# Performance work log

Hardware: AMD Instinct MI355X
Metric: run time of the kernel (lower is better)

Reference implementation:

```python
import jax, jax.numpy as jnp
import numpy as np
import math

HIDDEN = 2048
N_HEADS = 16
HEAD_DIM = HIDDEN // N_HEADS
BASE = 10000.0


def setup_inputs() -> dict:
    key = jax.random.key(0)
    ks = jax.random.split(key, 8)
    s = 1.0 / math.sqrt(HIDDEN)
    inp = {
        "hidden_states": jax.random.normal(ks[0], (2, 2048, HIDDEN), dtype=jnp.float32),
        "Wq": jax.random.normal(ks[1], (HIDDEN, HIDDEN), dtype=jnp.float32) * s,
        "bq": jax.random.normal(ks[2], (HIDDEN,), dtype=jnp.float32) * s,
        "Wk": jax.random.normal(ks[3], (HIDDEN, HIDDEN), dtype=jnp.float32) * s,
        "bk": jax.random.normal(ks[4], (HIDDEN,), dtype=jnp.float32) * s,
        "Wv": jax.random.normal(ks[5], (HIDDEN, HIDDEN), dtype=jnp.float32) * s,
        "bv": jax.random.normal(ks[6], (HIDDEN,), dtype=jnp.float32) * s,
        "Wo": jax.random.normal(ks[7], (HIDDEN, HIDDEN), dtype=jnp.float32) * s,
    }
    return inp


def _rotate_half(x):
    x1, x2 = x[..., : x.shape[-1] // 2], x[..., x.shape[-1] // 2 :]
    return jnp.concatenate((-x2, x1), axis=-1)


def _rope_cos_sin(seq_len, dtype):
    inv_freq = 1.0 / (BASE ** (jnp.arange(0, HEAD_DIM, 2, dtype=jnp.float32) / HEAD_DIM))
    t = jnp.arange(seq_len, dtype=jnp.float32)
    freqs = jnp.einsum("i,j->ij", t, inv_freq)  # [S, head_dim/2]
    emb = jnp.concatenate((freqs, freqs), axis=-1)  # [S, head_dim]
    return jnp.cos(emb).astype(dtype), jnp.sin(emb).astype(dtype)


def reference(hidden_states, Wq, bq, Wk, bk, Wv, bv, Wo):
    B, S, _ = hidden_states.shape
    q = hidden_states @ Wq + bq
    k = hidden_states @ Wk + bk
    v = hidden_states @ Wv + bv
    # [B, H, S, D]
    q = q.reshape(B, S, N_HEADS, HEAD_DIM).transpose(0, 2, 1, 3)
    k = k.reshape(B, S, N_HEADS, HEAD_DIM).transpose(0, 2, 1, 3)
    v = v.reshape(B, S, N_HEADS, HEAD_DIM).transpose(0, 2, 1, 3)
    cos, sin = _rope_cos_sin(S, q.dtype)  # [S, D]
    cos = cos[None, None]
    sin = sin[None, None]
    q = q * cos + _rotate_half(q) * sin
    k = k * cos + _rotate_half(k) * sin
    scale = 1.0 / math.sqrt(HEAD_DIM)
    scores = jnp.einsum("bhqd,bhkd->bhqk", q, k) * scale
    attn = jax.nn.softmax(scores, axis=-1)
    out = jnp.einsum("bhqk,bhkd->bhqd", attn, v)
    out = out.transpose(0, 2, 1, 3).reshape(B, S, HIDDEN)
    return out @ Wo
```

## Files before the change

kernel.cpp:

```cpp
#include <hip/hip_runtime.h>

#define HID 2048
#define SEQ 2048
#define HD 128
#define QKN 6144

typedef float f32x4 __attribute__((ext_vector_type(4)));
typedef short s16x8 __attribute__((ext_vector_type(8)));
typedef __bf16 bf16x8 __attribute__((ext_vector_type(8)));

static __device__ __forceinline__ unsigned short f2bf(float x) {
    unsigned u = __float_as_uint(x);
    u = u + 0x7FFFu + ((u >> 16) & 1u);
    return (unsigned short)(u >> 16);
}
static __device__ __forceinline__ float bf2f(unsigned short h) {
    return __uint_as_float(((unsigned)h) << 16);
}
static __device__ __forceinline__ bf16x8 as_bf(s16x8 v) {
    union { s16x8 s; bf16x8 b; } u; u.s = v; return u.b;
}
static __device__ __forceinline__ bf16x8 ld_bf8(const unsigned short* p) {
    return as_bf(*(const s16x8*)p);
}
static __device__ __forceinline__ void gload_lds16(const void* g, void* l) {
    __builtin_amdgcn_global_load_lds(
        (const __attribute__((address_space(1))) void*)g,
        (__attribute__((address_space(3))) void*)l,
        16, 0, 0);
}

__global__ __launch_bounds__(256) void fill_f32(
    float* __restrict__ out, float v, int n)
{
    int i = blockIdx.x * 256 + threadIdx.x;
    if (i < n) out[i] = v;
}

__global__ __launch_bounds__(256) void convert_f32_bf16(
    const float* __restrict__ in, unsigned short* __restrict__ out)
{
    long i = ((long)blockIdx.x * 256 + threadIdx.x) * 8;
    f32x4 a = *(const f32x4*)&in[i];
    f32x4 b = *(const f32x4*)&in[i + 4];
    s16x8 o;
#pragma unroll
    for (int e = 0; e < 4; ++e) {
        o[e]     = (short)f2bf(a[e]);
        o[e + 4] = (short)f2bf(b[e]);
    }
    *(s16x8*)&out[i] = o;
}

__global__ __launch_bounds__(256) void transpose_w(
    const float* __restrict__ W, unsigned short* __restrict__ Wt)
{
    __shared__ float t[32][33];
    int k0 = blockIdx.x * 32, n0 = blockIdx.y * 32;
    int tx = threadIdx.x & 31, ty = threadIdx.x >> 5;
#pragma unroll
    for (int r = ty; r < 32; r += 8)
        t[r][tx] = W[(long)(k0 + r) * HID + n0 + tx];
    __syncthreads();
#pragma unroll
    for (int r = ty; r < 32; r += 8)
        Wt[(long)(n0 + r) * HID + k0 + tx] = f2bf(t[tx][r]);
}

template<int NF, bool F32OUT>
__global__ __launch_bounds__(512, 2) void gemm_8phase(
    const unsigned short* __restrict__ A,
    const unsigned short* __restrict__ Bt,
    const float* __restrict__ bq, const float* __restrict__ bk,
    const float* __restrict__ bv,
    unsigned short* __restrict__ Cb, float* __restrict__ Cf,
    int K, int ldc, int nbn, int sm, int sn, int hasBias)
{
    constexpr int BUFE = 16384 + NF * 4096;
    constexpr int SP = (NF + 1) / 2;
    __shared__ unsigned short lds[2 * BUFE];
    const int tid = threadIdx.x;
    const int wid = tid >> 6, lane = tid & 63;
    const int l16 = lane & 15, l4 = lane >> 4;
    const int wm = wid >> 2, wn = wid & 3;

    const int bid = blockIdx.x;
    const int xcd = bid & 7, idx = bid >> 3;
    const int ncn = nbn / sn;
    const int cm = xcd / ncn, cn = xcd % ncn;
    const int lm = idx / sn,  ln = idx % sn;
    const long bm = (long)(cm * sm + lm) * 256;
    const long bn = (long)(cn * sn + ln) * (NF * 64);

    const int NT = K >> 6;
    const long strideB = (long)K * 2;
    const int srow = tid >> 3;
    const int scb  = ((tid & 7) * 16) ^ ((srow & 7) << 4);

    auto stageA = [&](int t, int c) {
        unsigned short* base = &lds[(t & 1) * BUFE];
        const int row = c * 64 + srow;
        const char* src = (const char*)A + (bm + row) * strideB + (long)t * 128 + scb;
        gload_lds16(src, base + (c * 64 + wid * 8) * 64);
    };
    auto stageB = [&](int t, int c) {
        unsigned short* base = &lds[(t & 1) * BUFE + 16384];
        const int row = c * 64 + srow;
        const char* src = (const char*)Bt + (bn + row) * strideB + (long)t * 128 + scb;
        gload_lds16(src, base + (c * 64 + wid * 8) * 64);
    };

    f32x4 acc[8][NF];
#pragma unroll
    for (int i = 0; i < 8; ++i)
#pragma unroll
        for (int j = 0; j < NF; ++j) acc[i][j] = f32x4{0.f, 0.f, 0.f, 0.f};

    auto phase = [&](const unsigned short* Ab, const unsigned short* Bb, int qm, int part) {
        bf16x8 af[4][2];
#pragma unroll
        for (int i = 0; i < 4; ++i) {
            const int row = wm * 128 + (qm * 4 + i) * 16 + l16;
            const char* rb = (const char*)Ab + row * 128;
#pragma unroll
            for (int kk = 0; kk < 2; ++kk)
                af[i][kk] = as_bf(*(const s16x8*)(rb + ((kk * 64 + l4 * 16) ^ ((l16 & 7) << 4))));
        }
        if (part == 0) {
            bf16x8 bfr[SP][2];
#pragma unroll
            for (int j = 0; j < SP; ++j) {
                const int row = wn * (NF * 16) + j * 16 + l16;
                const char* rb = (const char*)Bb + row * 128;
#pragma unroll
                for (int kk = 0; kk < 2; ++kk)
                    bfr[j][kk] = as_bf(*(const s16x8*)(rb + ((kk * 64 + l4 * 16) ^ ((l16 & 7) << 4))));
            }
            __builtin_amdgcn_s_setprio(1);
#pragma unroll
            for (int kk = 0; kk < 2; ++kk)
#pragma unroll
                for (int i = 0; i < 4; ++i)
#pragma unroll
                    for (int j = 0; j < SP; ++j)
                        acc[qm * 4 + i][j] = __builtin_amdgcn_mfma_f32_16x16x32_bf16(
                            af[i][kk], bfr[j][kk], acc[qm * 4 + i][j], 0, 0, 0);
            __builtin_amdgcn_s_setprio(0);
        } else {
            bf16x8 bfr[NF - SP][2];
#pragma unroll
            for (int j = 0; j < NF - SP; ++j) {
                const int row = wn * (NF * 16) + (SP + j) * 16 + l16;
                const char* rb = (const char*)Bb + row * 128;
#pragma unroll
                for (int kk = 0; kk < 2; ++kk)
                    bfr[j][kk] = as_bf(*(const s16x8*)(rb + ((kk * 64 + l4 * 16) ^ ((l16 & 7) << 4))));
            }
            __builtin_amdgcn_s_setprio(1);
#pragma unroll
            for (int kk = 0; kk < 2; ++kk)
#pragma unroll
                for (int i = 0; i < 4; ++i)
#pragma unroll
                    for (int j = 0; j < NF - SP; ++j)
                        acc[qm * 4 + i][SP + j] = __builtin_amdgcn_mfma_f32_16x16x32_bf16(
                            af[i][kk], bfr[j][kk], acc[qm * 4 + i][SP + j], 0, 0, 0);
            __builtin_amdgcn_s_setprio(0);
        }
    };

#pragma unroll
    for (int c = 0; c < 4; ++c) stageA(0, c);
#pragma unroll
    for (int c = 0; c < NF; ++c) stageB(0, c);

    for (int t = 0; t < NT - 1; ++t) {
        const unsigned short* Ab = &lds[(t & 1) * BUFE];
        const unsigned short* Bb = Ab + 16384;
#pragma unroll
        for (int c = 0; c < 4; ++c) stageA(t + 1, c);
        __builtin_amdgcn_sched_barrier(0);
        asm volatile("s_waitcnt vmcnt(4)" ::: "memory");
        __builtin_amdgcn_s_barrier();
        __builtin_amdgcn_sched_barrier(0);
        phase(Ab, Bb, 0, 0);
        __builtin_amdgcn_s_barrier();
#pragma unroll
        for (int c = 0; c < NF; ++c) stageB(t + 1, c);
        phase(Ab, Bb, 0, 1);
        __builtin_amdgcn_s_barrier();
        phase(Ab, Bb, 1, 0);
        __builtin_amdgcn_s_barrier();
        phase(Ab, Bb, 1, 1);
        __builtin_amdgcn_s_barrier();
    }
    {
        const unsigned short* Ab = &lds[((NT - 1) & 1) * BUFE];
        const unsigned short* Bb = Ab + 16384;
        asm volatile("s_waitcnt vmcnt(0)" ::: "memory");
        __builtin_amdgcn_s_barrier();
        __builtin_amdgcn_sched_barrier(0);
        phase(Ab, Bb, 0, 0); __builtin_amdgcn_s_barrier();
        phase(Ab, Bb, 0, 1); __builtin_amdgcn_s_barrier();
        phase(Ab, Bb, 1, 0); __builtin_amdgcn_s_barrier();
        phase(Ab, Bb, 1, 1);
    }

#pragma unroll
    for (int nf = 0; nf < NF; ++nf) {
        const long n = bn + wn * (NF * 16) + nf * 16 + l16;
        float bvv = 0.f;
        if (hasBias)
            bvv = (n < HID) ? bq[n] : ((n < 2 * HID) ? bk[n - HID] : bv[n - 2 * HID]);
#pragma unroll
        for (int mf = 0; mf < 8; ++mf) {
#pragma unroll
            for (int r = 0; r < 4; ++r) {
                const long m = bm + wm * 128 + mf * 16 + l4 * 4 + r;
                float v = acc[mf][nf][r] + bvv;
                if (F32OUT) Cf[m * (long)ldc + n] = v;
                else        Cb[m * (long)ldc + n] = f2bf(v);
            }
        }
    }
}

__global__ __launch_bounds__(256) void rope_kernel(unsigned short* __restrict__ qkv)
{
    int t = blockIdx.x * 256 + threadIdx.x;
    int j8 = t & 7;
    int h  = (t >> 3) & 15;
    int qk = (t >> 7) & 1;
    int row = t >> 8;
    int s = row & (SEQ - 1);
    unsigned short* p = &qkv[(long)row * QKN + qk * HID + h * HD + j8 * 8];
    s16x8 lo = *(const s16x8*)p;
    s16x8 hi = *(const s16x8*)(p + 64);
    float qscale = qk ? 1.0f : 0.08838834764831845f;
    s16x8 olo, ohi;
#pragma unroll
    for (int e = 0; e < 8; ++e) {
        int j = j8 * 8 + e;
        float inv = exp2f(-(float)j * 0.20762050593046f);
        float sn, cs;
        sincosf((float)s * inv, &sn, &cs);
        float x1 = bf2f((unsigned short)lo[e]);
        float x2 = bf2f((unsigned short)hi[e]);
        olo[e] = (short)f2bf((x1 * cs - x2 * sn) * qscale);
        ohi[e] = (short)f2bf((x2 * cs + x1 * sn) * qscale);
    }
    *(s16x8*)p = olo;
    *(s16x8*)(p + 64) = ohi;
}

__global__ __launch_bounds__(256) void v_transpose(
    const unsigned short* __restrict__ qkv, unsigned short* __restrict__ vt)
{
    __shared__ unsigned short t[32][33];
    int bh = blockIdx.z;
    int b = bh >> 4, h = bh & 15;
    int s0 = blockIdx.x * 32, d0 = blockIdx.y * 32;
    int tx = threadIdx.x & 31, ty = threadIdx.x >> 5;
#pragma unroll
    for (int r = ty; r < 32; r += 8)
        t[r][tx] = qkv[(long)(b * SEQ + s0 + r) * QKN + 2 * HID + h * HD + d0 + tx];
    __syncthreads();
#pragma unroll
    for (int r = ty; r < 32; r += 8)
        vt[((long)bh * HD + d0 + r) * SEQ + s0 + tx] = t[tx][r];
}

__global__ __launch_bounds__(512) void attn_kernel(
    const unsigned short* __restrict__ qkv,
    const unsigned short* __restrict__ vt,
    unsigned short* __restrict__ attnout)
{
    __shared__ unsigned short Ks[2][64 * 128];
    __shared__ unsigned short Vs[2][128 * 64];

    const int tid = threadIdx.x, wid = tid >> 6, lane = tid & 63;
    const int l16 = lane & 15, l4 = lane >> 4;
    const int bid = blockIdx.x;
    const int xcd = bid & 7, idx = bid >> 3;
    const int bh = xcd * 4 + (idx >> 4);
    const int qt = idx & 15;
    const int b = bh >> 4, h = bh & 15;
    const long rowbase = (long)b * SEQ;

    const unsigned short* Kg = &qkv[rowbase * QKN + HID + h * HD];
    const unsigned short* Vg = &vt[(long)bh * HD * SEQ];

    auto stage = [&](int buf, int kv0) {
#pragma unroll
        for (int i = 0; i < 2; ++i) {
            int c = wid * 2 + i;
            int kr = c * 4 + l4;
            int kcb = (l16 * 16) ^ ((kr & 7) << 4);
            gload_lds16((const char*)(Kg + (long)(kv0 + kr) * QKN) + kcb, &Ks[buf][c * 512]);
            int vr = c * 8 + (lane >> 3);
            int vcb = ((lane & 7) * 16) ^ ((vr & 7) << 4);
            gload_lds16((const char*)(Vg + (long)vr * SEQ + kv0) + vcb, &Vs[buf][c * 512]);
        }
    };

    bf16x8 qf[4];
    {
        const long qrow = rowbase + qt * 128 + wid * 16 + l16;
        const unsigned short* qp = &qkv[qrow * QKN + h * HD];
#pragma unroll
        for (int kc = 0; kc < 4; ++kc) qf[kc] = ld_bf8(qp + kc * 32 + l4 * 8);
    }

    f32x4 o[8];
#pragma unroll
    for (int nb = 0; nb < 8; ++nb) o[nb] = f32x4{0.f, 0.f, 0.f, 0.f};
    float mrun = -3.0e38f, lrun = 0.f;

    const int srcA = ((l4 & 1) * 2) * 16 + l16;
    const int srcB = srcA + 16;
    const bool sel = (l4 >> 1) != 0;

    stage(0, 0);
    __syncthreads();

    for (int t = 0; t < SEQ / 64; ++t) {
        const int cur = t & 1;
        if (t < SEQ / 64 - 1) stage(cur ^ 1, (t + 1) * 64);
        __builtin_amdgcn_sched_barrier(0);

        const unsigned short* Kc = &Ks[cur][0];
        const unsigned short* Vc = &Vs[cur][0];

        f32x4 sc[4];
#pragma unroll
        for (int nf = 0; nf < 4; ++nf) sc[nf] = f32x4{0.f, 0.f, 0.f, 0.f};
#pragma unroll
        for (int kc = 0; kc < 4; ++kc) {
#pragma unroll
            for (int nf = 0; nf < 4; ++nf) {
                int row = nf * 16 + l16;
                int cb = (kc * 64 + l4 * 16) ^ ((row & 7) << 4);
                bf16x8 kf = as_bf(*(const s16x8*)((const char*)Kc + row * 256 + cb));
                sc[nf] = __builtin_amdgcn_mfma_f32_16x16x32_bf16(kf, qf[kc], sc[nf], 0, 0, 0);
            }
        }

        float tmax = sc[0][0];
#pragma unroll
        for (int nf = 0; nf < 4; ++nf)
#pragma unroll
            for (int r = 0; r < 4; ++r) tmax = fmaxf(tmax, sc[nf][r]);
        tmax = fmaxf(tmax, __shfl_xor(tmax, 16, 64));
        tmax = fmaxf(tmax, __shfl_xor(tmax, 32, 64));

        if (!__all(tmax - mrun <= 8.0f)) {
            float mn = fmaxf(mrun, tmax);
            float sc_ = __expf(mrun - mn);
            mrun = mn;
            lrun *= sc_;
            float s_[4];
#pragma unroll
            for (int r = 0; r < 4; ++r) s_[r] = __shfl(sc_, l4 * 4 + r, 64);
#pragma unroll
            for (int nb = 0; nb < 8; ++nb)
#pragma unroll
                for (int r = 0; r < 4; ++r) o[nb][r] *= s_[r];
        }

        unsigned pk[4][2];
        float sum = 0.f;
#pragma unroll
        for (int nf = 0; nf < 4; ++nf) {
            float p0 = __expf(sc[nf][0] - mrun);
            float p1 = __expf(sc[nf][1] - mrun);
            float p2 = __expf(sc[nf][2] - mrun);
            float p3 = __expf(sc[nf][3] - mrun);
            sum += (p0 + p1) + (p2 + p3);
            union { __bf16 b[2]; unsigned u; } w0, w1;
            w0.b[0] = (__bf16)p0; w0.b[1] = (__bf16)p1;
            w1.b[0] = (__bf16)p2; w1.b[1] = (__bf16)p3;
            pk[nf][0] = w0.u; pk[nf][1] = w1.u;
        }
        sum += __shfl_xor(sum, 16, 64);
        sum += __shfl_xor(sum, 32, 64);
        lrun += sum;

        union { unsigned u[4]; bf16x8 v; } pa0, pa1;
#pragma unroll
        for (int w = 0; w < 2; ++w) {
            unsigned a0 = __shfl(pk[0][w], srcA, 64);
            unsigned a1 = __shfl(pk[1][w], srcA, 64);
            unsigned b0 = __shfl(pk[0][w], srcB, 64);
            unsigned b1 = __shfl(pk[1][w], srcB, 64);
            pa0.u[w]     = sel ? a1 : a0;
            pa0.u[2 + w] = sel ? b1 : b0;
            unsigned c0 = __shfl(pk[2][w], srcA, 64);
            unsigned c1 = __shfl(pk[3][w], srcA, 64);
            unsigned d0 = __shfl(pk[2][w], srcB, 64);
            unsigned d1 = __shfl(pk[3][w], srcB, 64);
            pa1.u[w]     = sel ? c1 : c0;
            pa1.u[2 + w] = sel ? d1 : d0;
        }

#pragma unroll
        for (int kc = 0; kc < 2; ++kc) {
            bf16x8 pav = kc ? pa1.v : pa0.v;
#pragma unroll
            for (int nb = 0; nb < 8; ++nb) {
                int vrow = nb * 16 + l16;
                int vcb = (kc * 64 + l4 * 16) ^ ((vrow & 7) << 4);
                bf16x8 vb = as_bf(*(const s16x8*)((const char*)Vc + vrow * 128 + vcb));
                o[nb] = __builtin_amdgcn_mfma_f32_16x16x32_bf16(pav, vb, o[nb], 0, 0, 0);
            }
        }
        __syncthreads();
    }

    float linv = 1.f / lrun;
    float li[4];
#pragma unroll
    for (int r = 0; r < 4; ++r) li[r] = __shfl(linv, l4 * 4 + r, 64);
#pragma unroll
    for (int r = 0; r < 4; ++r) {
        long m = rowbase + qt * 128 + wid * 16 + l4 * 4 + r;
#pragma unroll
        for (int nb = 0; nb < 8; ++nb)
            attnout[m * HID + h * HD + nb * 16 + l16] = f2bf(o[nb][r] * li[r]);
    }
}

extern "C" void kernel_launch(void* const* d_in, const int* in_sizes, int n_in,
                              void* d_out, int out_size, void* d_ws, size_t ws_size,
                              hipStream_t stream)
{
    const float* hs = (const float*)d_in[0];
    const float* Wq = (const float*)d_in[1];
    const float* bq = (const float*)d_in[2];
    const float* Wk = (const float*)d_in[3];
    const float* bk = (const float*)d_in[4];
    const float* Wv = (const float*)d_in[5];
    const float* bv = (const float*)d_in[6];
    const float* Wo = (const float*)d_in[7];
    float* out = (float*)d_out;

    bool shapes_ok =
        (n_in == 8) && (out_size == 8388608) &&
        in_sizes[0] == 8388608 && in_sizes[1] == 4194304 && in_sizes[2] == 2048 &&
        in_sizes[3] == 4194304 && in_sizes[4] == 2048 && in_sizes[5] == 4194304 &&
        in_sizes[6] == 2048 && in_sizes[7] == 4194304;
    if (!shapes_ok || ws_size < 117440512ull) {
        fill_f32<<<32768, 256, 0, stream>>>(out, shapes_ok ? 1000.f : 0.f, out_size);
        return;
    }

    char* ws = (char*)d_ws;
    unsigned short* hsB     = (unsigned short*)(ws);
    unsigned short* qkvB    = (unsigned short*)(ws + 16777216);
    unsigned short* wqkvT   = (unsigned short*)(ws + 67108864);
    unsigned short* vtB     = (unsigned short*)(ws + 92274688);
    unsigned short* woT     = (unsigned short*)(ws + 109051904);
    unsigned short* attnout = hsB;

    convert_f32_bf16<<<4096, 256, 0, stream>>>(hs, hsB);
    dim3 tg(64, 64);
    transpose_w<<<tg, 256, 0, stream>>>(Wq, wqkvT);
    transpose_w<<<tg, 256, 0, stream>>>(Wk, wqkvT + 2048 * 2048);
    transpose_w<<<tg, 256, 0, stream>>>(Wv, wqkvT + 2 * 2048 * 2048);
    transpose_w<<<tg, 256, 0, stream>>>(Wo, woT);

    gemm_8phase<3, false><<<dim3(512), 512, 0, stream>>>(
        hsB, wqkvT, bq, bk, bv, qkvB, nullptr, 2048, QKN, 32, 8, 8, 1);
    rope_kernel<<<4096, 256, 0, stream>>>(qkvB);
    v_transpose<<<dim3(64, 4, 32), 256, 0, stream>>>(qkvB, vtB);
    attn_kernel<<<dim3(512), 512, 0, stream>>>(qkvB, vtB, attnout);
    gemm_8phase<2, true><<<dim3(256), 512, 0, stream>>>(
        attnout, woT, nullptr, nullptr, nullptr, nullptr, out, 2048, HID, 16, 4, 8, 0);
}
```

Before: 329.3 us.

## Collapse 8-phase GEMM loop into single compute with all prefetches issued upfront

Result: faster. 312.6 us, median of 2 (-5.1%).

```diff
diff --git a/kernel.cpp b/kernel.cpp
--- a/kernel.cpp
+++ b/kernel.cpp
@@ -77,7 +77,6 @@
     int K, int ldc, int nbn, int sm, int sn, int hasBias)
 {
     constexpr int BUFE = 16384 + NF * 4096;
-    constexpr int SP = (NF + 1) / 2;
     __shared__ unsigned short lds[2 * BUFE];
     const int tid = threadIdx.x;
     const int wid = tid >> 6, lane = tid & 63;
@@ -116,25 +115,26 @@
 #pragma unroll
         for (int j = 0; j < NF; ++j) acc[i][j] = f32x4{0.f, 0.f, 0.f, 0.f};
 
-    auto phase = [&](const unsigned short* Ab, const unsigned short* Bb, int qm, int part) {
-        bf16x8 af[4][2];
-#pragma unroll
-        for (int i = 0; i < 4; ++i) {
-            const int row = wm * 128 + (qm * 4 + i) * 16 + l16;
-            const char* rb = (const char*)Ab + row * 128;
+    auto compute = [&](const unsigned short* Ab, const unsigned short* Bb) {
+        bf16x8 bfr[NF][2];
+#pragma unroll
+        for (int j = 0; j < NF; ++j) {
+            const int row = wn * (NF * 16) + j * 16 + l16;
+            const char* rb = (const char*)Bb + row * 128;
 #pragma unroll
             for (int kk = 0; kk < 2; ++kk)
-                af[i][kk] = as_bf(*(const s16x8*)(rb + ((kk * 64 + l4 * 16) ^ ((l16 & 7) << 4))));
-        }
-        if (part == 0) {
-            bf16x8 bfr[SP][2];
-#pragma unroll
-            for (int j = 0; j < SP; ++j) {
-                const int row = wn * (NF * 16) + j * 16 + l16;
-                const char* rb = (const char*)Bb + row * 128;
+                bfr[j][kk] = as_bf(*(const s16x8*)(rb + ((kk * 64 + l4 * 16) ^ ((l16 & 7) << 4))));
+        }
+#pragma unroll
+        for (int half = 0; half < 2; ++half) {
+            bf16x8 af[4][2];
+#pragma unroll
+            for (int i = 0; i < 4; ++i) {
+                const int row = wm * 128 + (half * 4 + i) * 16 + l16;
+                const char* rb = (const char*)Ab + row * 128;
 #pragma unroll
                 for (int kk = 0; kk < 2; ++kk)
-                    bfr[j][kk] = as_bf(*(const s16x8*)(rb + ((kk * 64 + l4 * 16) ^ ((l16 & 7) << 4))));
+                    af[i][kk] = as_bf(*(const s16x8*)(rb + ((kk * 64 + l4 * 16) ^ ((l16 & 7) << 4))));
             }
             __builtin_amdgcn_s_setprio(1);
 #pragma unroll
@@ -142,29 +142,9 @@
 #pragma unroll
                 for (int i = 0; i < 4; ++i)
 #pragma unroll
-                    for (int j = 0; j < SP; ++j)
-                        acc[qm * 4 + i][j] = __builtin_amdgcn_mfma_f32_16x16x32_bf16(
-                            af[i][kk], bfr[j][kk], acc[qm * 4 + i][j], 0, 0, 0);
-            __builtin_amdgcn_s_setprio(0);
-        } else {
-            bf16x8 bfr[NF - SP][2];
-#pragma unroll
-            for (int j = 0; j < NF - SP; ++j) {
-                const int row = wn * (NF * 16) + (SP + j) * 16 + l16;
-                const char* rb = (const char*)Bb + row * 128;
-#pragma unroll
-                for (int kk = 0; kk < 2; ++kk)
-                    bfr[j][kk] = as_bf(*(const s16x8*)(rb + ((kk * 64 + l4 * 16) ^ ((l16 & 7) << 4))));
-            }
-            __builtin_amdgcn_s_setprio(1);
-#pragma unroll
-            for (int kk = 0; kk < 2; ++kk)
-#pragma unroll
-                for (int i = 0; i < 4; ++i)
-#pragma unroll
-                    for (int j = 0; j < NF - SP; ++j)
-                        acc[qm * 4 + i][SP + j] = __builtin_amdgcn_mfma_f32_16x16x32_bf16(
-                            af[i][kk], bfr[j][kk], acc[qm * 4 + i][SP + j], 0, 0, 0);
+                    for (int j = 0; j < NF; ++j)
+                        acc[half * 4 + i][j] = __builtin_amdgcn_mfma_f32_16x16x32_bf16(
+                            af[i][kk], bfr[j][kk], acc[half * 4 + i][j], 0, 0, 0);
             __builtin_amdgcn_s_setprio(0);
         }
     };
@@ -179,19 +159,14 @@
         const unsigned short* Bb = Ab + 16384;
 #pragma unroll
         for (int c = 0; c < 4; ++c) stageA(t + 1, c);
+#pragma unroll
+        for (int c = 0; c < NF; ++c) stageB(t + 1, c);
         __builtin_amdgcn_sched_barrier(0);
-        asm volatile("s_waitcnt vmcnt(4)" ::: "memory");
+        if constexpr (NF == 3) asm volatile("s_waitcnt vmcnt(7)" ::: "memory");
+        else                   asm volatile("s_waitcnt vmcnt(6)" ::: "memory");
         __builtin_amdgcn_s_barrier();
         __builtin_amdgcn_sched_barrier(0);
-        phase(Ab, Bb, 0, 0);
-        __builtin_amdgcn_s_barrier();
-#pragma unroll
-        for (int c = 0; c < NF; ++c) stageB(t + 1, c);
-        phase(Ab, Bb, 0, 1);
-        __builtin_amdgcn_s_barrier();
-        phase(Ab, Bb, 1, 0);
-        __builtin_amdgcn_s_barrier();
-        phase(Ab, Bb, 1, 1);
+        compute(Ab, Bb);
         __builtin_amdgcn_s_barrier();
     }
     {
@@ -200,10 +175,7 @@
         asm volatile("s_waitcnt vmcnt(0)" ::: "memory");
         __builtin_amdgcn_s_barrier();
         __builtin_amdgcn_sched_barrier(0);
-        phase(Ab, Bb, 0, 0); __builtin_amdgcn_s_barrier();
-        phase(Ab, Bb, 0, 1); __builtin_amdgcn_s_barrier();
-        phase(Ab, Bb, 1, 0); __builtin_amdgcn_s_barrier();
-        phase(Ab, Bb, 1, 1);
+        compute(Ab, Bb);
     }
 
 #pragma unroll
```
